# Kernel tuning notes

Hardware: AMD Instinct MI355X
Metric: run time of the kernel (lower is better)

The kernel has to match this reference:

```python
import math
import jax, jax.numpy as jnp
import numpy as np

EPS = 1e-5
NUM_HEADER = 2


def pos_encoding(C, T, dtype):
    i = jnp.arange(C)
    exp = -((i - (i % 2)).astype(dtype) / C)
    freqs = jnp.power(jnp.asarray(10000.0, dtype), exp)[:, None]      # [C,1]
    phases = ((i % 2).astype(dtype) * (np.pi / 2))[:, None]           # [C,1]
    pos = jnp.arange(T, dtype=dtype)[None, :]                         # [1,T]
    return jnp.sin(pos * freqs + phases)                              # [C,T]


def layernorm2d(x, g, b):
    # LayerNorm over (C,T) jointly, per batch element (nn.LayerNorm([C, length]))
    mu = jnp.mean(x, axis=(1, 2), keepdims=True)
    var = jnp.mean((x - mu) ** 2, axis=(1, 2), keepdims=True)
    return (x - mu) * jax.lax.rsqrt(var + EPS) * g[None] + b[None]


def dsconv(x, dw_w, dw_b, pw_w, pw_b):
    # depthwise conv1d (groups=C, 'same' padding for odd k) + pointwise 1x1
    C = x.shape[1]
    k = dw_w.shape[-1]
    y = jax.lax.conv_general_dilated(
        x, dw_w[:, None, :], (1,), [(k // 2, k // 2)],
        dimension_numbers=('NCH', 'OIH', 'NCH'), feature_group_count=C)
    y = y + dw_b[None, :, None]
    y = jnp.einsum('bct,oc->bot', y, pw_w) + pw_b[None, :, None]
    return y


def attention(x, mask, Wq, Wk, Wv, Wo):
    # Faithful to source bug: all heads use Wqs[1]/Wks[1]/Wvs[1] -> identical heads.
    xt = jnp.transpose(x, (0, 2, 1))          # [B,T,C]
    C = xt.shape[-1]
    dk = C / NUM_HEADER
    q = xt @ Wq                               # [B,T,dk]
    k_ = xt @ Wk
    v = xt @ Wv
    s = jnp.einsum('bqd,bkd->bqk', q, k_) * (1.0 / math.sqrt(dk))
    hmask = mask[:, None, :]                  # mask over keys
    s = s * hmask + (1 - hmask) * (-1e30)
    a = jax.nn.softmax(s, axis=2) * mask[:, :, None]
    head = a @ v                              # [B,T,dk]
    heads = jnp.tile(head, (1, 1, NUM_HEADER))  # concat of identical heads
    out = heads @ Wo                          # [B,T,C]
    return jnp.transpose(out, (0, 2, 1))      # [B,C,T]


def setup_inputs() -> dict:
    key = jax.random.key(0)
    B, C, T = 16, 128, 1024
    NCONV, K = 4, 7
    dk = C // NUM_HEADER
    ks = jax.random.split(key, 12)
    inp = {
        'x': jax.random.normal(ks[0], (B, C, T), jnp.float32),
        'mask': jnp.ones((B, T), jnp.float32),
        'dw_w': jax.random.normal(ks[1], (NCONV, C, K), jnp.float32) * math.sqrt(2.0 / K),
        'dw_b': jnp.zeros((NCONV, C), jnp.float32),
        'pw_w': jax.random.normal(ks[2], (NCONV, C, C), jnp.float32) * math.sqrt(2.0 / C),
        'pw_b': jnp.zeros((NCONV, C), jnp.float32),
        'norm0_g': jnp.ones((C, T), jnp.float32),
        'norm0_b': jnp.zeros((C, T), jnp.float32),
        'norms_g': jnp.ones((NCONV, C, T), jnp.float32),
        'norms_b': jnp.zeros((NCONV, C, T), jnp.float32),
        'norme_g': jnp.ones((C, T), jnp.float32),
        'norme_b': jnp.zeros((C, T), jnp.float32),
        'Wq': jax.random.normal(ks[3], (C, dk), jnp.float32) * math.sqrt(2.0 / (C + dk)),
        'Wk': jax.random.normal(ks[4], (C, dk), jnp.float32) * math.sqrt(2.0 / (C + dk)),
        'Wv': jax.random.normal(ks[5], (C, dk), jnp.float32) * math.sqrt(2.0 / (C + dk)),
        'Wo': jax.random.normal(ks[6], (C, C), jnp.float32) * math.sqrt(2.0 / C),
        'fc_w': jax.random.normal(ks[7], (C, C), jnp.float32) * (0.1 * math.sqrt(6.0 / (2 * C))),
        'fc_b': jnp.zeros((C,), jnp.float32),
    }
    return inp


def reference(x, mask, dw_w, dw_b, pw_w, pw_b, norm0_g, norm0_b,
              norms_g, norms_b, norme_g, norme_b,
              Wq, Wk, Wv, Wo, fc_w, fc_b):
    B, C, T = x.shape
    nconv = dw_w.shape[0]
    # dropout is identity in eval mode (reference is deterministic)
    out = x + pos_encoding(C, T, x.dtype)[None]
    res = layernorm2d(out, norm0_g, norm0_b)
    for i in range(nconv):
        out = dsconv(out, dw_w[i], dw_b[i], pw_w[i], pw_b[i])
        out = jax.nn.relu(out)
        out = out + res
        res = out
        out = layernorm2d(out, norms_g[i], norms_b[i])
    out = attention(out, mask, Wq, Wk, Wv, Wo)
    out = out + res
    res = out
    out = layernorm2d(out, norme_g, norme_b)
    out = jnp.einsum('bct,oc->bot', out, fc_w) + fc_b[None, :, None]
    out = jax.nn.relu(out)
    out = out + res
    return out
```

## Files before the change

### kernel.cpp

```cpp
#include <hip/hip_runtime.h>
#include <math.h>

#define BB 16
#define CC 128
#define TT 1024
#define KK 7
#define DK 64
#define NSPLIT 4

typedef float f32x4 __attribute__((ext_vector_type(4)));
typedef short s16x8 __attribute__((ext_vector_type(8)));

__device__ inline short f2bf(float f) {
  union { float f; unsigned u; } v; v.f = f;
  unsigned r = (v.u + 0x7FFFu + ((v.u >> 16) & 1u)) >> 16;
  return (short)r;
}

__device__ inline float bf2f(short s) {
  union { unsigned u; float f; } v;
  v.u = ((unsigned)(unsigned short)s) << 16;
  return v.f;
}

__device__ inline void block_partial_256(float s, float ss, float* dst) {
#pragma unroll
  for (int off = 32; off; off >>= 1) { s += __shfl_xor(s, off); ss += __shfl_xor(ss, off); }
  __shared__ float red[8];
  int w = threadIdx.x >> 6;
  if ((threadIdx.x & 63) == 0) { red[2 * w] = s; red[2 * w + 1] = ss; }
  __syncthreads();
  if (threadIdx.x == 0) {
    for (int i = 1; i < 4; ++i) { s += red[2 * i]; ss += red[2 * i + 1]; }
    dst[0] = s; dst[1] = ss;
  }
}

__device__ inline void ln_stats_from_parts(const float* part_batch, int n, float* sh) {
  if (threadIdx.x < 64) {
    float s = 0.f, ss = 0.f;
    for (int i = threadIdx.x; i < n; i += 64) { s += part_batch[2 * i]; ss += part_batch[2 * i + 1]; }
#pragma unroll
    for (int off = 32; off; off >>= 1) { s += __shfl_xor(s, off); ss += __shfl_xor(ss, off); }
    if (threadIdx.x == 0) {
      const float invN = 1.f / (float)(CC * TT);
      float mu = s * invN;
      sh[0] = mu;
      sh[1] = rsqrtf(ss * invN - mu * mu + 1e-5f);
    }
  }
  __syncthreads();
}

__global__ __launch_bounds__(256) void k_prep0(const float* __restrict__ pww,
                                               const float* __restrict__ Wq,
                                               const float* __restrict__ Wk,
                                               const float* __restrict__ Wv,
                                               const float* __restrict__ Wo,
                                               const float* __restrict__ fcw,
                                               const float* __restrict__ x,
                                               short* __restrict__ pwwb,
                                               short* __restrict__ wqkvb,
                                               short* __restrict__ wo2b,
                                               short* __restrict__ fcwb,
                                               float* __restrict__ part0) {
  if (blockIdx.x < 448) {
    int i = blockIdx.x * 256 + threadIdx.x;
    if (i < 65536) { pwwb[i] = f2bf(pww[i]); return; }
    i -= 65536;
    if (i < 24576) {
      int m = i >> 7, c = i & 127;
      int sel = m >> 6, d = m & 63;
      const float* srcp = sel == 0 ? Wq : (sel == 1 ? Wk : Wv);
      wqkvb[i] = f2bf(srcp[c * DK + d]);
      return;
    }
    i -= 24576;
    if (i < 8192) {
      int o = i >> 6, d = i & 63;
      wo2b[i] = f2bf(Wo[d * CC + o] + Wo[(d + 64) * CC + o]);
      return;
    }
    i -= 8192;
    fcwb[i] = f2bf(fcw[i]);
    return;
  }
  int w = threadIdx.x >> 6, lane = threadIdx.x & 63;
  int bc = (blockIdx.x - 448) * 4 + w;
  int c = bc & (CC - 1);
  float freq = expf(-((float)(c & ~1) * (1.f / (float)CC)) * 9.210340371976184f);
  float ph = (c & 1) ? 1.5707963267948966f : 0.f;
  const float* xr = x + (size_t)bc * TT;
  float s = 0.f, ss = 0.f;
#pragma unroll
  for (int k = 0; k < 4; ++k) {
    int t = (k * 64 + lane) * 4;
    float4 v = *(const float4*)(xr + t);
    v.x += sinf((float)(t + 0) * freq + ph);
    v.y += sinf((float)(t + 1) * freq + ph);
    v.z += sinf((float)(t + 2) * freq + ph);
    v.w += sinf((float)(t + 3) * freq + ph);
    s += v.x + v.y + v.z + v.w;
    ss += v.x * v.x + v.y * v.y + v.z * v.z + v.w * v.w;
  }
#pragma unroll
  for (int off = 32; off; off >>= 1) { s += __shfl_xor(s, off); ss += __shfl_xor(ss, off); }
  if (lane == 0) { part0[(size_t)bc * 2] = s; part0[(size_t)bc * 2 + 1] = ss; }
}

template <bool LN_IN, bool LN_RES, bool ADD_POS>
__global__ __launch_bounds__(256) void k_dsconv(const float* __restrict__ in,
                                                const float* __restrict__ lng,
                                                const float* __restrict__ lnb,
                                                const float* __restrict__ part_in, int npart,
                                                const float* __restrict__ dww,
                                                const float* __restrict__ dwb,
                                                const short* __restrict__ pwwb,
                                                const float* __restrict__ pwb,
                                                float* __restrict__ out,
                                                float* __restrict__ part_out) {
  int tile = blockIdx.x & 31, b = blockIdx.x >> 5;
  int t0 = tile * 32;
  __shared__ float stats[2];
  __shared__ float xs[CC][41];
  __shared__ float xr2[CC][33];
  __shared__ __align__(16) short Dt[32][136];
  ln_stats_from_parts(part_in + (size_t)b * npart * 2, npart, stats);
  float mu = stats[0], rs = stats[1];

  for (int i = threadIdx.x; i < CC * 10; i += 256) {
    int c = i / 10, q = i - c * 10;
    int tb = t0 - 4 + q * 4;
    const float* rowp = in + ((size_t)b * CC + c) * TT;
    float freq = 0.f, ph = 0.f;
    if (ADD_POS) {
      freq = expf(-((float)(c & ~1) * (1.f / (float)CC)) * 9.210340371976184f);
      ph = (c & 1) ? 1.5707963267948966f : 0.f;
    }
    float r0, r1, r2, r3, o0, o1, o2, o3;
    bool full = (tb >= 0) && (tb + 4 <= TT);
    if (full) {
      float4 v = *(const float4*)(rowp + tb);
      if (ADD_POS) {
        v.x += sinf((float)(tb + 0) * freq + ph);
        v.y += sinf((float)(tb + 1) * freq + ph);
        v.z += sinf((float)(tb + 2) * freq + ph);
        v.w += sinf((float)(tb + 3) * freq + ph);
      }
      r0 = v.x; r1 = v.y; r2 = v.z; r3 = v.w;
      o0 = r0; o1 = r1; o2 = r2; o3 = r3;
      if (LN_IN) {
        float4 g = *(const float4*)(lng + (size_t)c * TT + tb);
        float4 bv = *(const float4*)(lnb + (size_t)c * TT + tb);
        o0 = (r0 - mu) * rs * g.x + bv.x;
        o1 = (r1 - mu) * rs * g.y + bv.y;
        o2 = (r2 - mu) * rs * g.z + bv.z;
        o3 = (r3 - mu) * rs * g.w + bv.w;
      }
    } else {
      float rr[4], oo[4];
#pragma unroll
      for (int k = 0; k < 4; ++k) {
        int t = tb + k;
        bool inb = (t >= 0) && (t < TT);
        float rv = 0.f;
        if (inb) {
          rv = rowp[t];
          if (ADD_POS) rv += sinf((float)t * freq + ph);
        }
        rr[k] = rv;
        float ov = rv;
        if (LN_IN && inb)
          ov = (rv - mu) * rs * lng[(size_t)c * TT + t] + lnb[(size_t)c * TT + t];
        oo[k] = ov;
      }
      r0 = rr[0]; r1 = rr[1]; r2 = rr[2]; r3 = rr[3];
      o0 = oo[0]; o1 = oo[1]; o2 = oo[2]; o3 = oo[3];
    }
    if (LN_IN && q >= 1 && q <= 8) {
      int tl = (q - 1) * 4;
      xr2[c][tl] = r0; xr2[c][tl + 1] = r1; xr2[c][tl + 2] = r2; xr2[c][tl + 3] = r3;
    }
    int base = q * 4;
    xs[c][base] = o0; xs[c][base + 1] = o1; xs[c][base + 2] = o2; xs[c][base + 3] = o3;
  }
  __syncthreads();
  for (int i = threadIdx.x; i < 32 * CC; i += 256) {
    int t = i >> 7, c = i & 127;
    float a = dwb[c];
#pragma unroll
    for (int j = 0; j < KK; ++j) a += dww[c * KK + j] * xs[c][t + j + 1];
    Dt[t][c] = f2bf(a);
  }
  __syncthreads();

  int w = threadIdx.x >> 6, lane = threadIdx.x & 63;
  int lo = lane & 15, hi = lane >> 4;
  f32x4 acc[2][2];
#pragma unroll
  for (int mt = 0; mt < 2; ++mt)
#pragma unroll
    for (int nt = 0; nt < 2; ++nt) { acc[mt][nt][0] = 0.f; acc[mt][nt][1] = 0.f; acc[mt][nt][2] = 0.f; acc[mt][nt][3] = 0.f; }
#pragma unroll
  for (int ks = 0; ks < 4; ++ks) {
    s16x8 b0 = *(const s16x8*)&Dt[lo][ks * 32 + hi * 8];
    s16x8 b1 = *(const s16x8*)&Dt[16 + lo][ks * 32 + hi * 8];
    s16x8 a0 = *(const s16x8*)&pwwb[(size_t)(w * 32 + lo) * CC + ks * 32 + hi * 8];
    s16x8 a1 = *(const s16x8*)&pwwb[(size_t)(w * 32 + 16 + lo) * CC + ks * 32 + hi * 8];
    acc[0][0] = __builtin_amdgcn_mfma_f32_16x16x32_bf16(a0, b0, acc[0][0], 0, 0, 0);
    acc[0][1] = __builtin_amdgcn_mfma_f32_16x16x32_bf16(a0, b1, acc[0][1], 0, 0, 0);
    acc[1][0] = __builtin_amdgcn_mfma_f32_16x16x32_bf16(a1, b0, acc[1][0], 0, 0, 0);
    acc[1][1] = __builtin_amdgcn_mfma_f32_16x16x32_bf16(a1, b1, acc[1][1], 0, 0, 0);
  }

  float s = 0.f, ss = 0.f;
#pragma unroll
  for (int mt = 0; mt < 2; ++mt)
#pragma unroll
    for (int nt = 0; nt < 2; ++nt)
#pragma unroll
      for (int r = 0; r < 4; ++r) {
        int row = w * 32 + mt * 16 + hi * 4 + r;
        int tl = nt * 16 + lo;
        int t = t0 + tl;
        float v = acc[mt][nt][r] + pwb[row];
        v = v > 0.f ? v : 0.f;
        float rv;
        if (LN_RES) {
          float raw = xs[row][tl + 4];
          rv = (raw - mu) * rs * lng[row * TT + t] + lnb[row * TT + t];
        } else if (LN_IN) {
          rv = xr2[row][tl];
        } else {
          rv = xs[row][tl + 4];
        }
        v += rv;
        xr2[row][tl] = v;
        s += v; ss += v * v;
      }
  __syncthreads();
  for (int u = threadIdx.x; u < 1024; u += 256) {
    int c = u >> 3, q = u & 7;
    float4 o4;
    o4.x = xr2[c][q * 4]; o4.y = xr2[c][q * 4 + 1];
    o4.z = xr2[c][q * 4 + 2]; o4.w = xr2[c][q * 4 + 3];
    *(float4*)(out + ((size_t)b * CC + c) * TT + t0 + q * 4) = o4;
  }
  block_partial_256(s, ss, part_out + (size_t)blockIdx.x * 2);
}

__global__ __launch_bounds__(256) void k_qkv(const float* __restrict__ in,
                                             const float* __restrict__ lng,
                                             const float* __restrict__ lnb,
                                             const float* __restrict__ part_in,
                                             const short* __restrict__ wqkvb,
                                             short* __restrict__ q,
                                             short* __restrict__ k,
                                             short* __restrict__ vt) {
  int tile = blockIdx.x & 31, b = blockIdx.x >> 5;
  int t0 = tile * 32;
  __shared__ float stats[2];
  __shared__ __align__(16) short Dt[32][136];
  __shared__ __align__(16) short stgQ[32 * 64];
  __shared__ __align__(16) short stgK[32 * 64];
  __shared__ __align__(16) short stgV[64][40];
  ln_stats_from_parts(part_in + (size_t)b * 64, 32, stats);
  float mu = stats[0], rs = stats[1];
  for (int i = threadIdx.x; i < CC * 8; i += 256) {
    int c = i >> 3, qq = i & 7;
    int t = qq * 4;
    size_t off = (size_t)c * TT + t0 + t;
    float4 v = *(const float4*)(in + (size_t)b * CC * TT + off);
    float4 g = *(const float4*)(lng + off);
    float4 bb = *(const float4*)(lnb + off);
    Dt[t + 0][c] = f2bf((v.x - mu) * rs * g.x + bb.x);
    Dt[t + 1][c] = f2bf((v.y - mu) * rs * g.y + bb.y);
    Dt[t + 2][c] = f2bf((v.z - mu) * rs * g.z + bb.z);
    Dt[t + 3][c] = f2bf((v.w - mu) * rs * g.w + bb.w);
  }
  __syncthreads();

  int w = threadIdx.x >> 6, lane = threadIdx.x & 63;
  int lo = lane & 15, hi = lane >> 4;
  f32x4 acc[3][2];
#pragma unroll
  for (int mt = 0; mt < 3; ++mt)
#pragma unroll
    for (int nt = 0; nt < 2; ++nt) { acc[mt][nt][0] = 0.f; acc[mt][nt][1] = 0.f; acc[mt][nt][2] = 0.f; acc[mt][nt][3] = 0.f; }
#pragma unroll
  for (int ks = 0; ks < 4; ++ks) {
    s16x8 b0 = *(const s16x8*)&Dt[lo][ks * 32 + hi * 8];
    s16x8 b1 = *(const s16x8*)&Dt[16 + lo][ks * 32 + hi * 8];
#pragma unroll
    for (int mt = 0; mt < 3; ++mt) {
      s16x8 a = *(const s16x8*)&wqkvb[(size_t)(w * 48 + mt * 16 + lo) * CC + ks * 32 + hi * 8];
      acc[mt][0] = __builtin_amdgcn_mfma_f32_16x16x32_bf16(a, b0, acc[mt][0], 0, 0, 0);
      acc[mt][1] = __builtin_amdgcn_mfma_f32_16x16x32_bf16(a, b1, acc[mt][1], 0, 0, 0);
    }
  }
#pragma unroll
  for (int mt = 0; mt < 3; ++mt)
#pragma unroll
    for (int nt = 0; nt < 2; ++nt) {
      int m0 = w * 48 + mt * 16 + hi * 4;
      int tl = nt * 16 + lo;
      short pv[4];
#pragma unroll
      for (int j = 0; j < 4; ++j) pv[j] = f2bf(acc[mt][nt][j]);
      if (m0 < 64) {
        *(short4*)&stgQ[tl * 64 + m0] = make_short4(pv[0], pv[1], pv[2], pv[3]);
      } else if (m0 < 128) {
        *(short4*)&stgK[tl * 64 + (m0 - 64)] = make_short4(pv[0], pv[1], pv[2], pv[3]);
      } else {
        int d = m0 - 128;
#pragma unroll
        for (int j = 0; j < 4; ++j) stgV[d + j][tl] = pv[j];
      }
    }
  __syncthreads();
  {
    int t = threadIdx.x >> 3, ch = threadIdx.x & 7;
    *(s16x8*)(q + ((size_t)b * TT + t0 + t) * DK + ch * 8) = *(const s16x8*)&stgQ[t * 64 + ch * 8];
    *(s16x8*)(k + ((size_t)b * TT + t0 + t) * DK + ch * 8) = *(const s16x8*)&stgK[t * 64 + ch * 8];
    int d = threadIdx.x >> 2, cv = threadIdx.x & 3;
    *(s16x8*)(vt + ((size_t)b * DK + d) * TT + t0 + cv * 8) = *(const s16x8*)&stgV[d][cv * 8];
  }
}

__global__ __launch_bounds__(128) void k_attn(const short* __restrict__ qb,
                                              const short* __restrict__ kbuf,
                                              const short* __restrict__ vtb,
                                              const float* __restrict__ mask,
                                              short* __restrict__ pacch,
                                              float* __restrict__ pml) {
  int sp = blockIdx.x & (NSPLIT - 1);
  int qt = (blockIdx.x >> 2) & 31;
  int b = blockIdx.x >> 7;
  int w = threadIdx.x >> 6, lane = threadIdx.x & 63;
  int lo = lane & 15, hi = lane >> 4;

  __shared__ __align__(16) short ks[64][72];
  __shared__ __align__(16) short vt[64][72];
  __shared__ __align__(16) short ps[2][16][68];
  __shared__ float ms[64];

  const short* qp = qb + ((size_t)b * TT + qt * 32 + w * 16 + lo) * DK + hi * 8;
  s16x8 aq0 = *(const s16x8*)qp;
  s16x8 aq1 = *(const s16x8*)(qp + 32);

  f32x4 acc[4];
  float m_i[4], l_i[4];
#pragma unroll
  for (int r = 0; r < 4; ++r) {
    m_i[r] = -3.0e38f; l_i[r] = 0.f;
#pragma unroll
    for (int nt = 0; nt < 4; ++nt) acc[nt][r] = 0.f;
  }
  const float scale = 0.125f;

  for (int kb2 = sp * (TT / 64 / NSPLIT); kb2 < (sp + 1) * (TT / 64 / NSPLIT); ++kb2) {
    __syncthreads();
    for (int i = threadIdx.x; i < 512; i += 128) {
      int r = i >> 3, ch = i & 7;
      *(s16x8*)&ks[r][ch * 8] =
          *(const s16x8*)(kbuf + ((size_t)b * TT + kb2 * 64 + r) * DK + ch * 8);
      *(s16x8*)&vt[r][ch * 8] =
          *(const s16x8*)(vtb + ((size_t)b * DK + r) * TT + kb2 * 64 + ch * 8);
    }
    if (threadIdx.x < 64) ms[threadIdx.x] = mask[(size_t)b * TT + kb2 * 64 + threadIdx.x];
    __syncthreads();

    f32x4 sc[4];
#pragma unroll
    for (int nt = 0; nt < 4; ++nt) {
      f32x4 z; z[0] = 0.f; z[1] = 0.f; z[2] = 0.f; z[3] = 0.f;
      s16x8 bk0 = *(const s16x8*)&ks[nt * 16 + lo][hi * 8];
      s16x8 bk1 = *(const s16x8*)&ks[nt * 16 + lo][32 + hi * 8];
      z = __builtin_amdgcn_mfma_f32_16x16x32_bf16(aq0, bk0, z, 0, 0, 0);
      z = __builtin_amdgcn_mfma_f32_16x16x32_bf16(aq1, bk1, z, 0, 0, 0);
      sc[nt] = z;
    }
#pragma unroll
    for (int nt = 0; nt < 4; ++nt) {
      float mv = ms[nt * 16 + lo];
      float addv = (1.f - mv) * -1e30f;
#pragma unroll
      for (int r = 0; r < 4; ++r) sc[nt][r] = sc[nt][r] * scale * mv + addv;
    }
    float alpha[4];
#pragma unroll
    for (int r = 0; r < 4; ++r) {
      float m0 = fmaxf(fmaxf(sc[0][r], sc[1][r]), fmaxf(sc[2][r], sc[3][r]));
#pragma unroll
      for (int off = 1; off < 16; off <<= 1) m0 = fmaxf(m0, __shfl_xor(m0, off));
      float mn = fmaxf(m_i[r], m0);
      alpha[r] = __expf(m_i[r] - mn);
      m_i[r] = mn;
    }
    float psum[4] = {0.f, 0.f, 0.f, 0.f};
#pragma unroll
    for (int nt = 0; nt < 4; ++nt)
#pragma unroll
      for (int r = 0; r < 4; ++r) {
        float p = __expf(sc[nt][r] - m_i[r]);
        psum[r] += p;
        ps[w][hi * 4 + r][nt * 16 + lo] = f2bf(p);
      }
#pragma unroll
    for (int r = 0; r < 4; ++r) {
      float sum = psum[r];
#pragma unroll
      for (int off = 1; off < 16; off <<= 1) sum += __shfl_xor(sum, off);
      l_i[r] = l_i[r] * alpha[r] + sum;
    }
#pragma unroll
    for (int nt = 0; nt < 4; ++nt)
#pragma unroll
      for (int r = 0; r < 4; ++r) acc[nt][r] *= alpha[r];

    s16x8 ap0 = *(const s16x8*)&ps[w][lo][hi * 8];
    s16x8 ap1 = *(const s16x8*)&ps[w][lo][32 + hi * 8];
#pragma unroll
    for (int nt = 0; nt < 4; ++nt) {
      s16x8 bv0 = *(const s16x8*)&vt[nt * 16 + lo][hi * 8];
      s16x8 bv1 = *(const s16x8*)&vt[nt * 16 + lo][32 + hi * 8];
      acc[nt] = __builtin_amdgcn_mfma_f32_16x16x32_bf16(ap0, bv0, acc[nt], 0, 0, 0);
      acc[nt] = __builtin_amdgcn_mfma_f32_16x16x32_bf16(ap1, bv1, acc[nt], 0, 0, 0);
    }
  }
  __syncthreads();
  short* pc = &ks[0][0];
#pragma unroll
  for (int r = 0; r < 4; ++r) {
    int row = w * 16 + hi * 4 + r;
#pragma unroll
    for (int nt = 0; nt < 4; ++nt) pc[row * 64 + nt * 16 + lo] = f2bf(acc[nt][r]);
    if (lo == 0) {
      size_t mb = (((size_t)b * TT + qt * 32 + row) * NSPLIT + sp) * 2;
      pml[mb] = m_i[r];
      pml[mb + 1] = l_i[r];
    }
  }
  __syncthreads();
  for (int u = threadIdx.x; u < 256; u += 128) {
    int row = u >> 3, ch = u & 7;
    size_t pb = (((size_t)b * TT + qt * 32 + row) * NSPLIT + sp) * DK;
    *(s16x8*)(pacch + pb + ch * 8) = *(const s16x8*)&pc[row * 64 + ch * 8];
  }
}

__global__ __launch_bounds__(256) void k_attnout2(const short* __restrict__ pacch,
                                                  const float* __restrict__ pml,
                                                  const float* __restrict__ mask,
                                                  const short* __restrict__ wo2b,
                                                  const float* __restrict__ res,
                                                  float* __restrict__ out,
                                                  float* __restrict__ part_out) {
  int tile = blockIdx.x & 31, b = blockIdx.x >> 5;
  int t0 = tile * 32;
  __shared__ __align__(16) short Ht[32][72];
  __shared__ float ot[128][33];
  {
    int i = threadIdx.x;
    int tr = i >> 3, q = i & 7;
    size_t rb = (size_t)b * TT + t0 + tr;
    float m[NSPLIT], l[NSPLIT];
#pragma unroll
    for (int s = 0; s < NSPLIT; ++s) {
      m[s] = pml[(rb * NSPLIT + s) * 2];
      l[s] = pml[(rb * NSPLIT + s) * 2 + 1];
    }
    float M = fmaxf(fmaxf(m[0], m[1]), fmaxf(m[2], m[3]));
    float wgt[NSPLIT], L = 0.f;
#pragma unroll
    for (int s = 0; s < NSPLIT; ++s) { wgt[s] = __expf(m[s] - M); L += wgt[s] * l[s]; }
    float inv = mask[rb] / L;
    float o[8] = {0.f, 0.f, 0.f, 0.f, 0.f, 0.f, 0.f, 0.f};
#pragma unroll
    for (int s = 0; s < NSPLIT; ++s) {
      s16x8 pv = *(const s16x8*)(pacch + (rb * NSPLIT + s) * DK + q * 8);
#pragma unroll
      for (int j = 0; j < 8; ++j) o[j] += wgt[s] * bf2f(pv[j]);
    }
    short h[8];
#pragma unroll
    for (int j = 0; j < 8; ++j) h[j] = f2bf(o[j] * inv);
    *(s16x8*)&Ht[tr][q * 8] = *(const s16x8*)h;
  }
  __syncthreads();

  int w = threadIdx.x >> 6, lane = threadIdx.x & 63;
  int lo = lane & 15, hi = lane >> 4;
  f32x4 acc[2][2];
#pragma unroll
  for (int mt = 0; mt < 2; ++mt)
#pragma unroll
    for (int nt = 0; nt < 2; ++nt) { acc[mt][nt][0] = 0.f; acc[mt][nt][1] = 0.f; acc[mt][nt][2] = 0.f; acc[mt][nt][3] = 0.f; }
#pragma unroll
  for (int ks = 0; ks < 2; ++ks) {
    s16x8 b0 = *(const s16x8*)&Ht[lo][ks * 32 + hi * 8];
    s16x8 b1 = *(const s16x8*)&Ht[16 + lo][ks * 32 + hi * 8];
    s16x8 a0 = *(const s16x8*)&wo2b[(size_t)(w * 32 + lo) * DK + ks * 32 + hi * 8];
    s16x8 a1 = *(const s16x8*)&wo2b[(size_t)(w * 32 + 16 + lo) * DK + ks * 32 + hi * 8];
    acc[0][0] = __builtin_amdgcn_mfma_f32_16x16x32_bf16(a0, b0, acc[0][0], 0, 0, 0);
    acc[0][1] = __builtin_amdgcn_mfma_f32_16x16x32_bf16(a0, b1, acc[0][1], 0, 0, 0);
    acc[1][0] = __builtin_amdgcn_mfma_f32_16x16x32_bf16(a1, b0, acc[1][0], 0, 0, 0);
    acc[1][1] = __builtin_amdgcn_mfma_f32_16x16x32_bf16(a1, b1, acc[1][1], 0, 0, 0);
  }
  float s = 0.f, ss = 0.f;
#pragma unroll
  for (int mt = 0; mt < 2; ++mt)
#pragma unroll
    for (int nt = 0; nt < 2; ++nt)
#pragma unroll
      for (int r = 0; r < 4; ++r) {
        int row = w * 32 + mt * 16 + hi * 4 + r;
        int tl = nt * 16 + lo;
        size_t idx = ((size_t)b * CC + row) * TT + t0 + tl;
        float v = acc[mt][nt][r] + res[idx];
        ot[row][tl] = v;
        s += v; ss += v * v;
      }
  __syncthreads();
  for (int u = threadIdx.x; u < 1024; u += 256) {
    int c = u >> 3, q = u & 7;
    float4 o4;
    o4.x = ot[c][q * 4]; o4.y = ot[c][q * 4 + 1];
    o4.z = ot[c][q * 4 + 2]; o4.w = ot[c][q * 4 + 3];
    *(float4*)(out + ((size_t)b * CC + c) * TT + t0 + q * 4) = o4;
  }
  block_partial_256(s, ss, part_out + (size_t)blockIdx.x * 2);
}

__global__ __launch_bounds__(256) void k_fc(const float* __restrict__ in,
                                            const float* __restrict__ lng,
                                            const float* __restrict__ lnb,
                                            const float* __restrict__ part_in,
                                            const short* __restrict__ fcwb,
                                            const float* __restrict__ fb,
                                            float* __restrict__ out) {
  int tile = blockIdx.x & 31, b = blockIdx.x >> 5;
  int t0 = tile * 32;
  __shared__ float stats[2];
  __shared__ float xr2[CC][33];
  __shared__ __align__(16) short Dt[32][136];
  ln_stats_from_parts(part_in + (size_t)b * 64, 32, stats);
  float mu = stats[0], rs = stats[1];
  for (int i = threadIdx.x; i < CC * 8; i += 256) {
    int c = i >> 3, q = i & 7;
    int t = q * 4;
    size_t off = (size_t)c * TT + t0 + t;
    float4 v = *(const float4*)(in + (size_t)b * CC * TT + off);
    float4 g = *(const float4*)(lng + off);
    float4 bb = *(const float4*)(lnb + off);
    xr2[c][t] = v.x; xr2[c][t + 1] = v.y; xr2[c][t + 2] = v.z; xr2[c][t + 3] = v.w;
    Dt[t + 0][c] = f2bf((v.x - mu) * rs * g.x + bb.x);
    Dt[t + 1][c] = f2bf((v.y - mu) * rs * g.y + bb.y);
    Dt[t + 2][c] = f2bf((v.z - mu) * rs * g.z + bb.z);
    Dt[t + 3][c] = f2bf((v.w - mu) * rs * g.w + bb.w);
  }
  __syncthreads();

  int w = threadIdx.x >> 6, lane = threadIdx.x & 63;
  int lo = lane & 15, hi = lane >> 4;
  f32x4 acc[2][2];
#pragma unroll
  for (int mt = 0; mt < 2; ++mt)
#pragma unroll
    for (int nt = 0; nt < 2; ++nt) { acc[mt][nt][0] = 0.f; acc[mt][nt][1] = 0.f; acc[mt][nt][2] = 0.f; acc[mt][nt][3] = 0.f; }
#pragma unroll
  for (int ks = 0; ks < 4; ++ks) {
    s16x8 b0 = *(const s16x8*)&Dt[lo][ks * 32 + hi * 8];
    s16x8 b1 = *(const s16x8*)&Dt[16 + lo][ks * 32 + hi * 8];
    s16x8 a0 = *(const s16x8*)&fcwb[(size_t)(w * 32 + lo) * CC + ks * 32 + hi * 8];
    s16x8 a1 = *(const s16x8*)&fcwb[(size_t)(w * 32 + 16 + lo) * CC + ks * 32 + hi * 8];
    acc[0][0] = __builtin_amdgcn_mfma_f32_16x16x32_bf16(a0, b0, acc[0][0], 0, 0, 0);
    acc[0][1] = __builtin_amdgcn_mfma_f32_16x16x32_bf16(a0, b1, acc[0][1], 0, 0, 0);
    acc[1][0] = __builtin_amdgcn_mfma_f32_16x16x32_bf16(a1, b0, acc[1][0], 0, 0, 0);
    acc[1][1] = __builtin_amdgcn_mfma_f32_16x16x32_bf16(a1, b1, acc[1][1], 0, 0, 0);
  }
#pragma unroll
  for (int mt = 0; mt < 2; ++mt)
#pragma unroll
    for (int nt = 0; nt < 2; ++nt)
#pragma unroll
      for (int r = 0; r < 4; ++r) {
        int row = w * 32 + mt * 16 + hi * 4 + r;
        int tl = nt * 16 + lo;
        float v = acc[mt][nt][r] + fb[row];
        v = v > 0.f ? v : 0.f;
        xr2[row][tl] = v + xr2[row][tl];
      }
  __syncthreads();
  for (int u = threadIdx.x; u < 1024; u += 256) {
    int c = u >> 3, q = u & 7;
    float4 o4;
    o4.x = xr2[c][q * 4]; o4.y = xr2[c][q * 4 + 1];
    o4.z = xr2[c][q * 4 + 2]; o4.w = xr2[c][q * 4 + 3];
    *(float4*)(out + ((size_t)b * CC + c) * TT + t0 + q * 4) = o4;
  }
}

extern "C" void kernel_launch(void* const* d_in, const int* in_sizes, int n_in,
                              void* d_out, int out_size, void* d_ws, size_t ws_size,
                              hipStream_t stream) {
  const float* x    = (const float*)d_in[0];
  const float* mask = (const float*)d_in[1];
  const float* dww  = (const float*)d_in[2];
  const float* dwb  = (const float*)d_in[3];
  const float* pww  = (const float*)d_in[4];
  const float* pwb  = (const float*)d_in[5];
  const float* n0g  = (const float*)d_in[6];
  const float* n0b  = (const float*)d_in[7];
  const float* nsg  = (const float*)d_in[8];
  const float* nsb  = (const float*)d_in[9];
  const float* neg_ = (const float*)d_in[10];
  const float* neb  = (const float*)d_in[11];
  const float* Wq   = (const float*)d_in[12];
  const float* Wk   = (const float*)d_in[13];
  const float* Wv   = (const float*)d_in[14];
  const float* Wo   = (const float*)d_in[15];
  const float* fcw  = (const float*)d_in[16];
  const float* fcb  = (const float*)d_in[17];
  float* out = (float*)d_out;

  float* W = (float*)d_ws;
  const size_t NBCT = (size_t)BB * CC * TT;
  const size_t NBTD = (size_t)BB * TT * DK;
  const size_t CT = (size_t)CC * TT;
  float* O     = W;
  float* S     = W + NBCT;
  float* PART0 = W + 2 * NBCT;
  float* PARTS = PART0 + 4096;
  float* PML   = PARTS + 5 * 1024;
  short* QB    = (short*)(PML + (size_t)BB * TT * NSPLIT * 2);
  short* KB    = QB + NBTD;
  short* VT    = KB + NBTD;
  short* PACCH = VT + NBTD;
  short* PWWB  = PACCH + NBTD * NSPLIT;
  short* WQKVB = PWWB + 65536;
  short* WO2B  = WQKVB + 24576;
  short* FCWB  = WO2B + 8192;

  k_prep0<<<960, 256, 0, stream>>>(pww, Wq, Wk, Wv, Wo, fcw, x,
                                   PWWB, WQKVB, WO2B, FCWB, PART0);
  k_dsconv<false, true, true><<<BB * 32, 256, 0, stream>>>(
      x, n0g, n0b, PART0, 128, dww, dwb, PWWB, pwb, S, PARTS);
  k_dsconv<true, false, false><<<BB * 32, 256, 0, stream>>>(
      S, nsg + 0 * CT, nsb + 0 * CT, PARTS, 32,
      dww + 1 * CC * KK, dwb + 1 * CC, PWWB + 1 * CC * CC, pwb + 1 * CC, O, PARTS + 1024);
  k_dsconv<true, false, false><<<BB * 32, 256, 0, stream>>>(
      O, nsg + 1 * CT, nsb + 1 * CT, PARTS + 1024, 32,
      dww + 2 * CC * KK, dwb + 2 * CC, PWWB + 2 * CC * CC, pwb + 2 * CC, S, PARTS + 2048);
  k_dsconv<true, false, false><<<BB * 32, 256, 0, stream>>>(
      S, nsg + 2 * CT, nsb + 2 * CT, PARTS + 2048, 32,
      dww + 3 * CC * KK, dwb + 3 * CC, PWWB + 3 * CC * CC, pwb + 3 * CC, O, PARTS + 3072);
  k_qkv<<<BB * 32, 256, 0, stream>>>(O, nsg + 3 * CT, nsb + 3 * CT, PARTS + 3072,
                                     WQKVB, QB, KB, VT);
  k_attn<<<BB * 32 * NSPLIT, 128, 0, stream>>>(QB, KB, VT, mask, PACCH, PML);
  k_attnout2<<<BB * 32, 256, 0, stream>>>(PACCH, PML, mask, WO2B, O, S, PARTS + 4096);
  k_fc<<<BB * 32, 256, 0, stream>>>(S, neg_, neb, PARTS + 4096, FCWB, fcb, out);
}
```

Before: 192.7 us.

## Double block sizes to 512 threads and prefetch K/V tiles in attention

The dsconv, qkv, attnout and fc kernels move from 256 to 512 threads per block. Each wave now computes one 16-row MFMA tile instead of two, and the qkv kernel leaves the extra waves idle during its matmul. The attention kernel loads the next K/V tile into registers while computing on the current one, and attnout issues all partial-accumulator loads up front. The goal is more waves per tile to hide memory latency; the costs are higher register pressure per block, idle waves in qkv, and larger block-wide barriers.

Result: faster. 187.3 us (-2.8%).

```diff
diff --git a/kernel.cpp b/kernel.cpp
--- a/kernel.cpp
+++ b/kernel.cpp
@@ -23,18 +23,19 @@
   return v.f;
 }
 
-__device__ inline void block_partial_256(float s, float ss, float* dst) {
+__device__ inline void block_partial_512(float s, float ss, float* dst) {
 #pragma unroll
   for (int off = 32; off; off >>= 1) { s += __shfl_xor(s, off); ss += __shfl_xor(ss, off); }
-  __shared__ float red[8];
+  __shared__ float red[16];
   int w = threadIdx.x >> 6;
   if ((threadIdx.x & 63) == 0) { red[2 * w] = s; red[2 * w + 1] = ss; }
   __syncthreads();
   if (threadIdx.x == 0) {
-    for (int i = 1; i < 4; ++i) { s += red[2 * i]; ss += red[2 * i + 1]; }
+    for (int i = 1; i < 8; ++i) { s += red[2 * i]; ss += red[2 * i + 1]; }
     dst[0] = s; dst[1] = ss;
   }
 }
+
 
 __device__ inline void ln_stats_from_parts(const float* part_batch, int n, float* sh) {
   if (threadIdx.x < 64) {
@@ -109,7 +110,7 @@
 }
 
 template <bool LN_IN, bool LN_RES, bool ADD_POS>
-__global__ __launch_bounds__(256) void k_dsconv(const float* __restrict__ in,
+__global__ __launch_bounds__(512) void k_dsconv(const float* __restrict__ in,
                                                 const float* __restrict__ lng,
                                                 const float* __restrict__ lnb,
                                                 const float* __restrict__ part_in, int npart,
@@ -128,7 +129,7 @@
   ln_stats_from_parts(part_in + (size_t)b * npart * 2, npart, stats);
   float mu = stats[0], rs = stats[1];
 
-  for (int i = threadIdx.x; i < CC * 10; i += 256) {
+  for (int i = threadIdx.x; i < CC * 10; i += 512) {
     int c = i / 10, q = i - c * 10;
     int tb = t0 - 4 + q * 4;
     const float* rowp = in + ((size_t)b * CC + c) * TT;
@@ -185,7 +186,7 @@
     xs[c][base] = o0; xs[c][base + 1] = o1; xs[c][base + 2] = o2; xs[c][base + 3] = o3;
   }
   __syncthreads();
-  for (int i = threadIdx.x; i < 32 * CC; i += 256) {
+  for (int i = threadIdx.x; i < 32 * CC; i += 512) {
     int t = i >> 7, c = i & 127;
     float a = dwb[c];
 #pragma unroll
@@ -196,60 +197,53 @@
 
   int w = threadIdx.x >> 6, lane = threadIdx.x & 63;
   int lo = lane & 15, hi = lane >> 4;
-  f32x4 acc[2][2];
-#pragma unroll
-  for (int mt = 0; mt < 2; ++mt)
-#pragma unroll
-    for (int nt = 0; nt < 2; ++nt) { acc[mt][nt][0] = 0.f; acc[mt][nt][1] = 0.f; acc[mt][nt][2] = 0.f; acc[mt][nt][3] = 0.f; }
+  f32x4 acc[2];
+#pragma unroll
+  for (int nt = 0; nt < 2; ++nt) { acc[nt][0] = 0.f; acc[nt][1] = 0.f; acc[nt][2] = 0.f; acc[nt][3] = 0.f; }
 #pragma unroll
   for (int ks = 0; ks < 4; ++ks) {
     s16x8 b0 = *(const s16x8*)&Dt[lo][ks * 32 + hi * 8];
     s16x8 b1 = *(const s16x8*)&Dt[16 + lo][ks * 32 + hi * 8];
-    s16x8 a0 = *(const s16x8*)&pwwb[(size_t)(w * 32 + lo) * CC + ks * 32 + hi * 8];
-    s16x8 a1 = *(const s16x8*)&pwwb[(size_t)(w * 32 + 16 + lo) * CC + ks * 32 + hi * 8];
-    acc[0][0] = __builtin_amdgcn_mfma_f32_16x16x32_bf16(a0, b0, acc[0][0], 0, 0, 0);
-    acc[0][1] = __builtin_amdgcn_mfma_f32_16x16x32_bf16(a0, b1, acc[0][1], 0, 0, 0);
-    acc[1][0] = __builtin_amdgcn_mfma_f32_16x16x32_bf16(a1, b0, acc[1][0], 0, 0, 0);
-    acc[1][1] = __builtin_amdgcn_mfma_f32_16x16x32_bf16(a1, b1, acc[1][1], 0, 0, 0);
+    s16x8 a0 = *(const s16x8*)&pwwb[(size_t)(w * 16 + lo) * CC + ks * 32 + hi * 8];
+    acc[0] = __builtin_amdgcn_mfma_f32_16x16x32_bf16(a0, b0, acc[0], 0, 0, 0);
+    acc[1] = __builtin_amdgcn_mfma_f32_16x16x32_bf16(a0, b1, acc[1], 0, 0, 0);
   }
 
   float s = 0.f, ss = 0.f;
 #pragma unroll
-  for (int mt = 0; mt < 2; ++mt)
-#pragma unroll
-    for (int nt = 0; nt < 2; ++nt)
-#pragma unroll
-      for (int r = 0; r < 4; ++r) {
-        int row = w * 32 + mt * 16 + hi * 4 + r;
-        int tl = nt * 16 + lo;
-        int t = t0 + tl;
-        float v = acc[mt][nt][r] + pwb[row];
-        v = v > 0.f ? v : 0.f;
-        float rv;
-        if (LN_RES) {
-          float raw = xs[row][tl + 4];
-          rv = (raw - mu) * rs * lng[row * TT + t] + lnb[row * TT + t];
-        } else if (LN_IN) {
-          rv = xr2[row][tl];
-        } else {
-          rv = xs[row][tl + 4];
-        }
-        v += rv;
-        xr2[row][tl] = v;
-        s += v; ss += v * v;
-      }
-  __syncthreads();
-  for (int u = threadIdx.x; u < 1024; u += 256) {
+  for (int nt = 0; nt < 2; ++nt)
+#pragma unroll
+    for (int r = 0; r < 4; ++r) {
+      int row = w * 16 + hi * 4 + r;
+      int tl = nt * 16 + lo;
+      int t = t0 + tl;
+      float v = acc[nt][r] + pwb[row];
+      v = v > 0.f ? v : 0.f;
+      float rv;
+      if (LN_RES) {
+        float raw = xs[row][tl + 4];
+        rv = (raw - mu) * rs * lng[row * TT + t] + lnb[row * TT + t];
+      } else if (LN_IN) {
+        rv = xr2[row][tl];
+      } else {
+        rv = xs[row][tl + 4];
+      }
+      v += rv;
+      xr2[row][tl] = v;
+      s += v; ss += v * v;
+    }
+  __syncthreads();
+  for (int u = threadIdx.x; u < 1024; u += 512) {
     int c = u >> 3, q = u & 7;
     float4 o4;
     o4.x = xr2[c][q * 4]; o4.y = xr2[c][q * 4 + 1];
     o4.z = xr2[c][q * 4 + 2]; o4.w = xr2[c][q * 4 + 3];
     *(float4*)(out + ((size_t)b * CC + c) * TT + t0 + q * 4) = o4;
   }
-  block_partial_256(s, ss, part_out + (size_t)blockIdx.x * 2);
-}
-
-__global__ __launch_bounds__(256) void k_qkv(const float* __restrict__ in,
+  block_partial_512(s, ss, part_out + (size_t)blockIdx.x * 2);
+}
+
+__global__ __launch_bounds__(512) void k_qkv(const float* __restrict__ in,
                                              const float* __restrict__ lng,
                                              const float* __restrict__ lnb,
                                              const float* __restrict__ part_in,
@@ -266,7 +260,7 @@
   __shared__ __align__(16) short stgV[64][40];
   ln_stats_from_parts(part_in + (size_t)b * 64, 32, stats);
   float mu = stats[0], rs = stats[1];
-  for (int i = threadIdx.x; i < CC * 8; i += 256) {
+  for (int i = threadIdx.x; i < CC * 8; i += 512) {
     int c = i >> 3, qq = i & 7;
     int t = qq * 4;
     size_t off = (size_t)c * TT + t0 + t;
@@ -282,48 +276,55 @@
 
   int w = threadIdx.x >> 6, lane = threadIdx.x & 63;
   int lo = lane & 15, hi = lane >> 4;
-  f32x4 acc[3][2];
-#pragma unroll
-  for (int mt = 0; mt < 3; ++mt)
-#pragma unroll
-    for (int nt = 0; nt < 2; ++nt) { acc[mt][nt][0] = 0.f; acc[mt][nt][1] = 0.f; acc[mt][nt][2] = 0.f; acc[mt][nt][3] = 0.f; }
-#pragma unroll
-  for (int ks = 0; ks < 4; ++ks) {
-    s16x8 b0 = *(const s16x8*)&Dt[lo][ks * 32 + hi * 8];
-    s16x8 b1 = *(const s16x8*)&Dt[16 + lo][ks * 32 + hi * 8];
-#pragma unroll
-    for (int mt = 0; mt < 3; ++mt) {
-      s16x8 a = *(const s16x8*)&wqkvb[(size_t)(w * 48 + mt * 16 + lo) * CC + ks * 32 + hi * 8];
-      acc[mt][0] = __builtin_amdgcn_mfma_f32_16x16x32_bf16(a, b0, acc[mt][0], 0, 0, 0);
-      acc[mt][1] = __builtin_amdgcn_mfma_f32_16x16x32_bf16(a, b1, acc[mt][1], 0, 0, 0);
-    }
-  }
-#pragma unroll
-  for (int mt = 0; mt < 3; ++mt)
-#pragma unroll
-    for (int nt = 0; nt < 2; ++nt) {
-      int m0 = w * 48 + mt * 16 + hi * 4;
-      int tl = nt * 16 + lo;
-      short pv[4];
-#pragma unroll
-      for (int j = 0; j < 4; ++j) pv[j] = f2bf(acc[mt][nt][j]);
-      if (m0 < 64) {
-        *(short4*)&stgQ[tl * 64 + m0] = make_short4(pv[0], pv[1], pv[2], pv[3]);
-      } else if (m0 < 128) {
-        *(short4*)&stgK[tl * 64 + (m0 - 64)] = make_short4(pv[0], pv[1], pv[2], pv[3]);
-      } else {
-        int d = m0 - 128;
-#pragma unroll
-        for (int j = 0; j < 4; ++j) stgV[d + j][tl] = pv[j];
-      }
-    }
+  if (w < 6) {
+    f32x4 acc[2][2];
+#pragma unroll
+    for (int mt = 0; mt < 2; ++mt)
+#pragma unroll
+      for (int nt = 0; nt < 2; ++nt) { acc[mt][nt][0] = 0.f; acc[mt][nt][1] = 0.f; acc[mt][nt][2] = 0.f; acc[mt][nt][3] = 0.f; }
+#pragma unroll
+    for (int ks = 0; ks < 4; ++ks) {
+      s16x8 b0 = *(const s16x8*)&Dt[lo][ks * 32 + hi * 8];
+      s16x8 b1 = *(const s16x8*)&Dt[16 + lo][ks * 32 + hi * 8];
+#pragma unroll
+      for (int mt = 0; mt < 2; ++mt) {
+        s16x8 a = *(const s16x8*)&wqkvb[(size_t)(w * 32 + mt * 16 + lo) * CC + ks * 32 + hi * 8];
+        acc[mt][0] = __builtin_amdgcn_mfma_f32_16x16x32_bf16(a, b0, acc[mt][0], 0, 0, 0);
+        acc[mt][1] = __builtin_amdgcn_mfma_f32_16x16x32_bf16(a, b1, acc[mt][1], 0, 0, 0);
+      }
+    }
+#pragma unroll
+    for (int mt = 0; mt < 2; ++mt)
+#pragma unroll
+      for (int nt = 0; nt < 2; ++nt) {
+        int m0 = w * 32 + mt * 16 + hi * 4;
+        int tl = nt * 16 + lo;
+        short pv[4];
+#pragma unroll
+        for (int j = 0; j < 4; ++j) pv[j] = f2bf(acc[mt][nt][j]);
+        if (m0 < 64) {
+          *(short4*)&stgQ[tl * 64 + m0] = make_short4(pv[0], pv[1], pv[2], pv[3]);
+        } else if (m0 < 128) {
+          *(short4*)&stgK[tl * 64 + (m0 - 64)] = make_short4(pv[0], pv[1], pv[2], pv[3]);
+        } else {
+          int d = m0 - 128;
+#pragma unroll
+          for (int j = 0; j < 4; ++j) stgV[d + j][tl] = pv[j];
+        }
+      }
+  }
   __syncthreads();
   {
-    int t = threadIdx.x >> 3, ch = threadIdx.x & 7;
-    *(s16x8*)(q + ((size_t)b * TT + t0 + t) * DK + ch * 8) = *(const s16x8*)&stgQ[t * 64 + ch * 8];
-    *(s16x8*)(k + ((size_t)b * TT + t0 + t) * DK + ch * 8) = *(const s16x8*)&stgK[t * 64 + ch * 8];
-    int d = threadIdx.x >> 2, cv = threadIdx.x & 3;
-    *(s16x8*)(vt + ((size_t)b * DK + d) * TT + t0 + cv * 8) = *(const s16x8*)&stgV[d][cv * 8];
+    if (threadIdx.x < 256) {
+      int t = threadIdx.x >> 3, ch = threadIdx.x & 7;
+      *(s16x8*)(q + ((size_t)b * TT + t0 + t) * DK + ch * 8) = *(const s16x8*)&stgQ[t * 64 + ch * 8];
+      int d = threadIdx.x >> 2, cv = threadIdx.x & 3;
+      *(s16x8*)(vt + ((size_t)b * DK + d) * TT + t0 + cv * 8) = *(const s16x8*)&stgV[d][cv * 8];
+    } else {
+      int i = threadIdx.x - 256;
+      int t = i >> 3, ch = i & 7;
+      *(s16x8*)(k + ((size_t)b * TT + t0 + t) * DK + ch * 8) = *(const s16x8*)&stgK[t * 64 + ch * 8];
+    }
   }
 }
 
@@ -357,18 +358,38 @@
     for (int nt = 0; nt < 4; ++nt) acc[nt][r] = 0.f;
   }
   const float scale = 0.125f;
-
-  for (int kb2 = sp * (TT / 64 / NSPLIT); kb2 < (sp + 1) * (TT / 64 / NSPLIT); ++kb2) {
+  const int kb0 = sp * (TT / 64 / NSPLIT);
+
+  s16x8 kreg[4], vreg[4];
+#pragma unroll
+  for (int j = 0; j < 4; ++j) {
+    int i = threadIdx.x + j * 128;
+    int r = i >> 3, ch = i & 7;
+    kreg[j] = *(const s16x8*)(kbuf + ((size_t)b * TT + kb0 * 64 + r) * DK + ch * 8);
+    vreg[j] = *(const s16x8*)(vtb + ((size_t)b * DK + r) * TT + kb0 * 64 + ch * 8);
+  }
+
+  for (int it = 0; it < 4; ++it) {
+    int kb2 = kb0 + it;
     __syncthreads();
-    for (int i = threadIdx.x; i < 512; i += 128) {
+#pragma unroll
+    for (int j = 0; j < 4; ++j) {
+      int i = threadIdx.x + j * 128;
       int r = i >> 3, ch = i & 7;
-      *(s16x8*)&ks[r][ch * 8] =
-          *(const s16x8*)(kbuf + ((size_t)b * TT + kb2 * 64 + r) * DK + ch * 8);
-      *(s16x8*)&vt[r][ch * 8] =
-          *(const s16x8*)(vtb + ((size_t)b * DK + r) * TT + kb2 * 64 + ch * 8);
+      *(s16x8*)&ks[r][ch * 8] = kreg[j];
+      *(s16x8*)&vt[r][ch * 8] = vreg[j];
     }
     if (threadIdx.x < 64) ms[threadIdx.x] = mask[(size_t)b * TT + kb2 * 64 + threadIdx.x];
     __syncthreads();
+    if (it < 3) {
+#pragma unroll
+      for (int j = 0; j < 4; ++j) {
+        int i = threadIdx.x + j * 128;
+        int r = i >> 3, ch = i & 7;
+        kreg[j] = *(const s16x8*)(kbuf + ((size_t)b * TT + (kb2 + 1) * 64 + r) * DK + ch * 8);
+        vreg[j] = *(const s16x8*)(vtb + ((size_t)b * DK + r) * TT + (kb2 + 1) * 64 + ch * 8);
+      }
+    }
 
     f32x4 sc[4];
 #pragma unroll
@@ -449,7 +470,7 @@
   }
 }
 
-__global__ __launch_bounds__(256) void k_attnout2(const short* __restrict__ pacch,
+__global__ __launch_bounds__(512) void k_attnout2(const short* __restrict__ pacch,
                                                   const float* __restrict__ pml,
                                                   const float* __restrict__ mask,
                                                   const short* __restrict__ wo2b,
@@ -460,10 +481,14 @@
   int t0 = tile * 32;
   __shared__ __align__(16) short Ht[32][72];
   __shared__ float ot[128][33];
-  {
+  if (threadIdx.x < 256) {
     int i = threadIdx.x;
     int tr = i >> 3, q = i & 7;
     size_t rb = (size_t)b * TT + t0 + tr;
+    s16x8 pvv[NSPLIT];
+#pragma unroll
+    for (int s = 0; s < NSPLIT; ++s)
+      pvv[s] = *(const s16x8*)(pacch + (rb * NSPLIT + s) * DK + q * 8);
     float m[NSPLIT], l[NSPLIT];
 #pragma unroll
     for (int s = 0; s < NSPLIT; ++s) {
@@ -478,9 +503,8 @@
     float o[8] = {0.f, 0.f, 0.f, 0.f, 0.f, 0.f, 0.f, 0.f};
 #pragma unroll
     for (int s = 0; s < NSPLIT; ++s) {
-      s16x8 pv = *(const s16x8*)(pacch + (rb * NSPLIT + s) * DK + q * 8);
-#pragma unroll
-      for (int j = 0; j < 8; ++j) o[j] += wgt[s] * bf2f(pv[j]);
+#pragma unroll
+      for (int j = 0; j < 8; ++j) o[j] += wgt[s] * bf2f(pvv[s][j]);
     }
     short h[8];
 #pragma unroll
@@ -491,48 +515,41 @@
 
   int w = threadIdx.x >> 6, lane = threadIdx.x & 63;
   int lo = lane & 15, hi = lane >> 4;
-  f32x4 acc[2][2];
-#pragma unroll
-  for (int mt = 0; mt < 2; ++mt)
-#pragma unroll
-    for (int nt = 0; nt < 2; ++nt) { acc[mt][nt][0] = 0.f; acc[mt][nt][1] = 0.f; acc[mt][nt][2] = 0.f; acc[mt][nt][3] = 0.f; }
+  f32x4 acc[2];
+#pragma unroll
+  for (int nt = 0; nt < 2; ++nt) { acc[nt][0] = 0.f; acc[nt][1] = 0.f; acc[nt][2] = 0.f; acc[nt][3] = 0.f; }
 #pragma unroll
   for (int ks = 0; ks < 2; ++ks) {
     s16x8 b0 = *(const s16x8*)&Ht[lo][ks * 32 + hi * 8];
     s16x8 b1 = *(const s16x8*)&Ht[16 + lo][ks * 32 + hi * 8];
-    s16x8 a0 = *(const s16x8*)&wo2b[(size_t)(w * 32 + lo) * DK + ks * 32 + hi * 8];
-    s16x8 a1 = *(const s16x8*)&wo2b[(size_t)(w * 32 + 16 + lo) * DK + ks * 32 + hi * 8];
-    acc[0][0] = __builtin_amdgcn_mfma_f32_16x16x32_bf16(a0, b0, acc[0][0], 0, 0, 0);
-    acc[0][1] = __builtin_amdgcn_mfma_f32_16x16x32_bf16(a0, b1, acc[0][1], 0, 0, 0);
-    acc[1][0] = __builtin_amdgcn_mfma_f32_16x16x32_bf16(a1, b0, acc[1][0], 0, 0, 0);
-    acc[1][1] = __builtin_amdgcn_mfma_f32_16x16x32_bf16(a1, b1, acc[1][1], 0, 0, 0);
+    s16x8 a0 = *(const s16x8*)&wo2b[(size_t)(w * 16 + lo) * DK + ks * 32 + hi * 8];
+    acc[0] = __builtin_amdgcn_mfma_f32_16x16x32_bf16(a0, b0, acc[0], 0, 0, 0);
+    acc[1] = __builtin_amdgcn_mfma_f32_16x16x32_bf16(a0, b1, acc[1], 0, 0, 0);
   }
   float s = 0.f, ss = 0.f;
 #pragma unroll
-  for (int mt = 0; mt < 2; ++mt)
-#pragma unroll
-    for (int nt = 0; nt < 2; ++nt)
-#pragma unroll
-      for (int r = 0; r < 4; ++r) {
-        int row = w * 32 + mt * 16 + hi * 4 + r;
-        int tl = nt * 16 + lo;
-        size_t idx = ((size_t)b * CC + row) * TT + t0 + tl;
-        float v = acc[mt][nt][r] + res[idx];
-        ot[row][tl] = v;
-        s += v; ss += v * v;
-      }
-  __syncthreads();
-  for (int u = threadIdx.x; u < 1024; u += 256) {
+  for (int nt = 0; nt < 2; ++nt)
+#pragma unroll
+    for (int r = 0; r < 4; ++r) {
+      int row = w * 16 + hi * 4 + r;
+      int tl = nt * 16 + lo;
+      size_t idx = ((size_t)b * CC + row) * TT + t0 + tl;
+      float v = acc[nt][r] + res[idx];
+      ot[row][tl] = v;
+      s += v; ss += v * v;
+    }
+  __syncthreads();
+  for (int u = threadIdx.x; u < 1024; u += 512) {
     int c = u >> 3, q = u & 7;
     float4 o4;
     o4.x = ot[c][q * 4]; o4.y = ot[c][q * 4 + 1];
     o4.z = ot[c][q * 4 + 2]; o4.w = ot[c][q * 4 + 3];
     *(float4*)(out + ((size_t)b * CC + c) * TT + t0 + q * 4) = o4;
   }
-  block_partial_256(s, ss, part_out + (size_t)blockIdx.x * 2);
-}
-
-__global__ __launch_bounds__(256) void k_fc(const float* __restrict__ in,
+  block_partial_512(s, ss, part_out + (size_t)blockIdx.x * 2);
+}
+
+__global__ __launch_bounds__(512) void k_fc(const float* __restrict__ in,
                                             const float* __restrict__ lng,
                                             const float* __restrict__ lnb,
                                             const float* __restrict__ part_in,
@@ -546,7 +563,7 @@
   __shared__ __align__(16) short Dt[32][136];
   ln_stats_from_parts(part_in + (size_t)b * 64, 32, stats);
   float mu = stats[0], rs = stats[1];
-  for (int i = threadIdx.x; i < CC * 8; i += 256) {
+  for (int i = threadIdx.x; i < CC * 8; i += 512) {
     int c = i >> 3, q = i & 7;
     int t = q * 4;
     size_t off = (size_t)c * TT + t0 + t;
@@ -563,36 +580,29 @@
 
   int w = threadIdx.x >> 6, lane = threadIdx.x & 63;
   int lo = lane & 15, hi = lane >> 4;
-  f32x4 acc[2][2];
-#pragma unroll
-  for (int mt = 0; mt < 2; ++mt)
-#pragma unroll
-    for (int nt = 0; nt < 2; ++nt) { acc[mt][nt][0] = 0.f; acc[mt][nt][1] = 0.f; acc[mt][nt][2] = 0.f; acc[mt][nt][3] = 0.f; }
+  f32x4 acc[2];
+#pragma unroll
+  for (int nt = 0; nt < 2; ++nt) { acc[nt][0] = 0.f; acc[nt][1] = 0.f; acc[nt][2] = 0.f; acc[nt][3] = 0.f; }
 #pragma unroll
   for (int ks = 0; ks < 4; ++ks) {
     s16x8 b0 = *(const s16x8*)&Dt[lo][ks * 32 + hi * 8];
     s16x8 b1 = *(const s16x8*)&Dt[16 + lo][ks * 32 + hi * 8];
-    s16x8 a0 = *(const s16x8*)&fcwb[(size_t)(w * 32 + lo) * CC + ks * 32 + hi * 8];
-    s16x8 a1 = *(const s16x8*)&fcwb[(size_t)(w * 32 + 16 + lo) * CC + ks * 32 + hi * 8];
-    acc[0][0] = __builtin_amdgcn_mfma_f32_16x16x32_bf16(a0, b0, acc[0][0], 0, 0, 0);
-    acc[0][1] = __builtin_amdgcn_mfma_f32_16x16x32_bf16(a0, b1, acc[0][1], 0, 0, 0);
-    acc[1][0] = __builtin_amdgcn_mfma_f32_16x16x32_bf16(a1, b0, acc[1][0], 0, 0, 0);
-    acc[1][1] = __builtin_amdgcn_mfma_f32_16x16x32_bf16(a1, b1, acc[1][1], 0, 0, 0);
-  }
-#pragma unroll
-  for (int mt = 0; mt < 2; ++mt)
-#pragma unroll
-    for (int nt = 0; nt < 2; ++nt)
-#pragma unroll
-      for (int r = 0; r < 4; ++r) {
-        int row = w * 32 + mt * 16 + hi * 4 + r;
-        int tl = nt * 16 + lo;
-        float v = acc[mt][nt][r] + fb[row];
-        v = v > 0.f ? v : 0.f;
-        xr2[row][tl] = v + xr2[row][tl];
-      }
-  __syncthreads();
-  for (int u = threadIdx.x; u < 1024; u += 256) {
+    s16x8 a0 = *(const s16x8*)&fcwb[(size_t)(w * 16 + lo) * CC + ks * 32 + hi * 8];
+    acc[0] = __builtin_amdgcn_mfma_f32_16x16x32_bf16(a0, b0, acc[0], 0, 0, 0);
+    acc[1] = __builtin_amdgcn_mfma_f32_16x16x32_bf16(a0, b1, acc[1], 0, 0, 0);
+  }
+#pragma unroll
+  for (int nt = 0; nt < 2; ++nt)
+#pragma unroll
+    for (int r = 0; r < 4; ++r) {
+      int row = w * 16 + hi * 4 + r;
+      int tl = nt * 16 + lo;
+      float v = acc[nt][r] + fb[row];
+      v = v > 0.f ? v : 0.f;
+      xr2[row][tl] = v + xr2[row][tl];
+    }
+  __syncthreads();
+  for (int u = threadIdx.x; u < 1024; u += 512) {
     int c = u >> 3, q = u & 7;
     float4 o4;
     o4.x = xr2[c][q * 4]; o4.y = xr2[c][q * 4 + 1];
@@ -644,20 +654,20 @@
 
   k_prep0<<<960, 256, 0, stream>>>(pww, Wq, Wk, Wv, Wo, fcw, x,
                                    PWWB, WQKVB, WO2B, FCWB, PART0);
-  k_dsconv<false, true, true><<<BB * 32, 256, 0, stream>>>(
+  k_dsconv<false, true, true><<<BB * 32, 512, 0, stream>>>(
       x, n0g, n0b, PART0, 128, dww, dwb, PWWB, pwb, S, PARTS);
-  k_dsconv<true, false, false><<<BB * 32, 256, 0, stream>>>(
+  k_dsconv<true, false, false><<<BB * 32, 512, 0, stream>>>(
       S, nsg + 0 * CT, nsb + 0 * CT, PARTS, 32,
       dww + 1 * CC * KK, dwb + 1 * CC, PWWB + 1 * CC * CC, pwb + 1 * CC, O, PARTS + 1024);
-  k_dsconv<true, false, false><<<BB * 32, 256, 0, stream>>>(
+  k_dsconv<true, false, false><<<BB * 32, 512, 0, stream>>>(
       O, nsg + 1 * CT, nsb + 1 * CT, PARTS + 1024, 32,
       dww + 2 * CC * KK, dwb + 2 * CC, PWWB + 2 * CC * CC, pwb + 2 * CC, S, PARTS + 2048);
-  k_dsconv<true, false, false><<<BB * 32, 256, 0, stream>>>(
+  k_dsconv<true, false, false><<<BB * 32, 512, 0, stream>>>(
       S, nsg + 2 * CT, nsb + 2 * CT, PARTS + 2048, 32,
       dww + 3 * CC * KK, dwb + 3 * CC, PWWB + 3 * CC * CC, pwb + 3 * CC, O, PARTS + 3072);
-  k_qkv<<<BB * 32, 256, 0, stream>>>(O, nsg + 3 * CT, nsb + 3 * CT, PARTS + 3072,
+  k_qkv<<<BB * 32, 512, 0, stream>>>(O, nsg + 3 * CT, nsb + 3 * CT, PARTS + 3072,
                                      WQKVB, QB, KB, VT);
   k_attn<<<BB * 32 * NSPLIT, 128, 0, stream>>>(QB, KB, VT, mask, PACCH, PML);
-  k_attnout2<<<BB * 32, 256, 0, stream>>>(PACCH, PML, mask, WO2B, O, S, PARTS + 4096);
-  k_fc<<<BB * 32, 256, 0, stream>>>(S, neg_, neb, PARTS + 4096, FCWB, fcb, out);
-}
+  k_attnout2<<<BB * 32, 512, 0, stream>>>(PACCH, PML, mask, WO2B, O, S, PARTS + 4096);
+  k_fc<<<BB * 32, 512, 0, stream>>>(S, neg_, neb, PARTS + 4096, FCWB, fcb, out);
+}
```
